# Kernel tuning notes

Hardware: AMD Instinct MI355X
Metric: run time of the kernel (lower is better)

## Reference

```python
import jax, jax.numpy as jnp
import numpy as np

C_REG = 0.1
MAX_ITER = 15
SIGMA = 0.1  # centering parameter for the interior-point steps


def _qp_solve(G, e, h, A, b, max_iter):
    """Batched primal-dual interior-point solver (fixed iteration count, as QPFunction(maxIter=...)).

    Solves per task: min_z 0.5 z^T G z + e^T z  s.t.  z <= h (inequality matrix is identity),  A z = b.
    G: (t,n,n), e,h: (t,n), A: (t,p,n), b: (t,p). Returns z: (t,n).
    """
    t, n = e.shape
    p = A.shape[1]
    dt = G.dtype
    z = jnp.zeros((t, n), dt)
    s = jnp.ones((t, n), dt)    # slack for z + s = h
    lam = jnp.ones((t, n), dt)  # inequality duals
    nu = jnp.zeros((t, p), dt)  # equality duals
    At = jnp.swapaxes(A, 1, 2)              # (t,n,p)
    eye_n = jnp.eye(n, dtype=dt)
    zeros_pp = jnp.zeros((t, p, p), dt)

    def step(carry, _):
        z, s, lam, nu = carry
        # KKT residuals (infeasible-start Newton)
        rz = jnp.einsum('bij,bj->bi', G, z) + e + lam + jnp.einsum('bpi,bp->bi', A, nu)
        rs = z + s - h
        ra = jnp.einsum('bpi,bi->bp', A, z) - b
        mu = jnp.mean(lam * s, axis=1, keepdims=True)
        # eliminate ds and dlam -> reduced saddle system in (dz, dnu)
        r1 = -rz - (lam * rs - lam * s + SIGMA * mu) / s
        D = lam / s  # diagonal of barrier Hessian contribution
        M_top = jnp.concatenate([G + D[:, :, None] * eye_n, At], axis=2)  # (t,n,n+p)
        M_bot = jnp.concatenate([A, zeros_pp], axis=2)                    # (t,p,n+p)
        M = jnp.concatenate([M_top, M_bot], axis=1)                       # (t,n+p,n+p)
        rhs = jnp.concatenate([r1, -ra], axis=1)
        sol = jnp.linalg.solve(M, rhs[..., None])[..., 0]
        dz, dnu = sol[:, :n], sol[:, n:]
        ds = -rs - dz
        dlam = (lam * dz + lam * rs - lam * s + SIGMA * mu) / s
        # fraction-to-boundary step size keeping s, lam > 0
        ratio_s = jnp.where(ds < 0, -s / ds, jnp.inf)
        ratio_l = jnp.where(dlam < 0, -lam / dlam, jnp.inf)
        alpha = jnp.minimum(1.0, 0.99 * jnp.minimum(ratio_s.min(axis=1), ratio_l.min(axis=1)))[:, None]
        return (z + alpha * dz, s + alpha * ds, lam + alpha * dlam, nu + alpha * dnu), None

    (z, s, lam, nu), _ = jax.lax.scan(step, (z, s, lam, nu), xs=None, length=max_iter)
    return z


def setup_inputs() -> dict:
    key = jax.random.key(0)
    k1, k2, k3 = jax.random.split(key, 3)
    tasks, n_way, n_shot, d = 64, 5, 15, 4096
    n_support = n_way * n_shot          # 75
    n_query = 150
    query = jax.random.normal(k1, (tasks, n_query, d), dtype=jnp.float32)
    support = jax.random.normal(k2, (tasks, n_support, d), dtype=jnp.float32)
    support_labels = jax.random.randint(k3, (tasks, n_support), 0, n_way)
    return {"query": query, "support": support, "support_labels": support_labels,
            "n_way": n_way, "n_shot": n_shot}


def reference(query, support, support_labels, n_way, n_shot):
    t, ns, d = support.shape
    nq = query.shape[1]
    n = ns * n_way
    dt = support.dtype
    # linear kernel Gram matrix on support: (t, ns, ns)
    K = jnp.einsum('bnd,bmd->bnm', support, support)
    # block kernel = K kron I_{n_way}, then + I (the module adds 1.0 * eye)
    I_w = jnp.eye(n_way, dtype=dt)
    block_K = (K[:, :, None, :, None] * I_w[None, None, :, None, :]).reshape(t, n, n)
    G = block_K + jnp.eye(n, dtype=dt)
    # one-hot labels, flattened to (t, ns*n_way)
    y1h = jax.nn.one_hot(support_labels, n_way, dtype=dt).reshape(t, n)
    e = -y1h
    h = C_REG * y1h
    # A = I_{ns} kron ones(1, n_way): sums duals over classes per support point
    A = jnp.tile(jnp.eye(ns, dtype=dt)[:, :, None], (1, 1, n_way)).reshape(ns, n)
    A = jnp.broadcast_to(A, (t, ns, n))
    b = jnp.zeros((t, ns), dt)
    z = _qp_solve(G, e, h, A, b, MAX_ITER)
    qp_sol = z.reshape(t, ns, n_way)
    # compatibility = support . query^T : (t, ns, nq); logits = sum over support
    compat = jnp.einsum('bnd,bqd->bnq', support, query)
    logits = jnp.einsum('bnq,bnw->bqw', compat, qp_sol)  # (t, nq, n_way)
    return logits
```

## Files before the change

### kernel.cpp

```cpp
#include <hip/hip_runtime.h>
#include <math.h>

#define T_TASKS 64
#define NS 75
#define NW 5
#define NTOT 375
#define NQ 150
#define DIM 4096
#define QP_ITERS 15
#define SIGMA 0.1f
#define CREG 0.1f

#define OFF_K   0u
#define OFF_W   369664u
#define OFF_Z   2417664u
#define OFF_S   2441664u
#define OFF_LAM 2465664u
#define OFF_NU  2489664u
#define OFF_TV  2494464u

__global__ void qp_init(float* __restrict__ z, float* __restrict__ s,
                        float* __restrict__ lam, float* __restrict__ nu) {
    int idx = blockIdx.x * 256 + threadIdx.x;
    if (idx < T_TASKS * NTOT) { z[idx] = 0.f; s[idx] = 1.f; lam[idx] = 1.f; }
    if (idx < T_TASKS * NS) nu[idx] = 0.f;
}

__global__ __launch_bounds__(256) void gram_partial(const float* __restrict__ support,
                                                    float* __restrict__ Kp) {
    int qd = blockIdx.x, b = blockIdx.y;
    __shared__ __align__(16) float Ss[80 * 132];
    int tid = threadIdx.x;
    int tx = tid & 15, ty = tid >> 4;
    float acc[5][5];
#pragma unroll
    for (int u = 0; u < 5; u++)
#pragma unroll
        for (int v = 0; v < 5; v++) acc[u][v] = 0.f;
    const float* sb = support + (size_t)b * NS * DIM + qd * 1024;
    for (int cc = 0; cc < 8; cc++) {
        __syncthreads();
        for (int idx = tid; idx < 80 * 32; idx += 256) {
            int r = idx >> 5, d4 = idx & 31;
            float4 v = make_float4(0.f, 0.f, 0.f, 0.f);
            if (r < 75) v = *(const float4*)&sb[(size_t)r * DIM + cc * 128 + d4 * 4];
            *(float4*)&Ss[r * 132 + d4 * 4] = v;
        }
        __syncthreads();
        for (int d4 = 0; d4 < 32; d4++) {
            float4 av[5], bv[5];
#pragma unroll
            for (int u = 0; u < 5; u++) av[u] = *(const float4*)&Ss[(ty * 5 + u) * 132 + d4 * 4];
#pragma unroll
            for (int v = 0; v < 5; v++) bv[v] = *(const float4*)&Ss[(tx * 5 + v) * 132 + d4 * 4];
#pragma unroll
            for (int u = 0; u < 5; u++)
#pragma unroll
                for (int v = 0; v < 5; v++)
                    acc[u][v] += av[u].x * bv[v].x + av[u].y * bv[v].y +
                                 av[u].z * bv[v].z + av[u].w * bv[v].w;
        }
    }
    float* Ko = Kp + (size_t)(qd * 64 + b) * 5776;
#pragma unroll
    for (int u = 0; u < 5; u++) {
        int row = ty * 5 + u;
#pragma unroll
        for (int v = 0; v < 5; v++) {
            int col = tx * 5 + v;
            if (row < 75 && col < 75) Ko[row * 76 + col] = acc[u][v];
        }
    }
}

__global__ void gram_reduce(const float* __restrict__ Kp, float* __restrict__ Kg) {
    int idx = blockIdx.x * 256 + threadIdx.x;
    if (idx >= 64 * 5776) return;
    int rc = idx % 5776;
    int row = rc / 76, col = rc % 76;
    float val;
    if (row < 75 && col < 75)
        val = Kp[idx] + Kp[369664 + idx] + Kp[2 * 369664 + idx] + Kp[3 * 369664 + idx];
    else
        val = (row == col) ? 1.f : 0.f;
    Kg[idx] = val;
}

__device__ __forceinline__ void reg_gj80(float (&M)[5][5],
                                         float (*prow)[80], float (*fcol)[80],
                                         int tx, int ty) {
    for (int k = 0; k < 75; k++) {
        int bf = k & 1;
        if (ty == (k & 15)) {
#pragma unroll
            for (int m = 0; m < 5; m++) {
                if (ty + 16 * m == k) {
#pragma unroll
                    for (int n = 0; n < 5; n++) prow[bf][tx + 16 * n] = M[m][n];
                }
            }
        }
        if (tx == (k & 15)) {
#pragma unroll
            for (int n = 0; n < 5; n++) {
                if (tx + 16 * n == k) {
#pragma unroll
                    for (int m = 0; m < 5; m++) fcol[bf][ty + 16 * m] = M[m][n];
                }
            }
        }
        __syncthreads();
        float pinv = 1.f / prow[bf][k];
        float pv[5], fv[5], ps[5];
#pragma unroll
        for (int n = 0; n < 5; n++) {
            pv[n] = prow[bf][tx + 16 * n];
            ps[n] = pv[n] * pinv;
        }
#pragma unroll
        for (int m = 0; m < 5; m++) {
            int r = ty + 16 * m;
            float f = fcol[bf][r] * pinv;
            fv[m] = (r == k) ? 0.f : f;
        }
#pragma unroll
        for (int m = 0; m < 5; m++) {
            int r = ty + 16 * m;
            bool rk = (r == k);
#pragma unroll
            for (int n = 0; n < 5; n++) {
                int c = tx + 16 * n;
                float val = M[m][n] - fv[m] * pv[n];
                val = rk ? ps[n] : val;
                val = (c == k) ? (rk ? pinv : -fv[m]) : val;
                M[m][n] = val;
            }
        }
    }
}

__global__ __launch_bounds__(256) void factor_kernel(
        const float* __restrict__ Kg, const int* __restrict__ labels,
        const float* __restrict__ zg, const float* __restrict__ sg,
        const float* __restrict__ lamg, const float* __restrict__ nug,
        float* __restrict__ Wg, float* __restrict__ tvg) {
    int w = blockIdx.x, b = blockIdx.y;
    int tid = threadIdx.x;
    int tx = tid & 15, ty = tid >> 4;
    __shared__ float prow[2][80], fcol[2][80];
    __shared__ float zw[80], r1w[80], Dv[80], swv[80], lwv[80], nuwv[80];
    __shared__ int labv[80];
    __shared__ float mred[4];

    float M[5][5];
    const float* Kt = Kg + (size_t)b * 5776;
#pragma unroll
    for (int m = 0; m < 5; m++) {
        int r = ty + 16 * m;
#pragma unroll
        for (int n = 0; n < 5; n++) {
            int c = tx + 16 * n;
            M[m][n] = (r < 76 && c < 76) ? Kt[r * 76 + c] : ((r == c) ? 1.f : 0.f);
        }
    }
    if (tid < 80) {
        float zv = 0.f, sv = 1.f, lv = 0.f, nv = 0.f; int lb = -1;
        if (tid < 75) {
            zv = zg[b * NTOT + tid * NW + w];
            sv = sg[b * NTOT + tid * NW + w];
            lv = lamg[b * NTOT + tid * NW + w];
            nv = nug[b * NS + tid];
            lb = labels[b * NS + tid];
        }
        zw[tid] = zv; swv[tid] = sv; lwv[tid] = lv; nuwv[tid] = nv; labv[tid] = lb;
    }
    float part = 0.f;
    for (int idx = tid; idx < NTOT; idx += 256)
        part += lamg[b * NTOT + idx] * sg[b * NTOT + idx];
#pragma unroll
    for (int off = 32; off > 0; off >>= 1) part += __shfl_xor(part, off, 64);
    if ((tid & 63) == 0) mred[tid >> 6] = part;
    __syncthreads();
    float mu = (mred[0] + mred[1] + mred[2] + mred[3]) * (1.f / (float)NTOT);

    float gp[5];
#pragma unroll
    for (int m = 0; m < 5; m++) {
        float a = 0.f;
#pragma unroll
        for (int n = 0; n < 5; n++) a += M[m][n] * zw[tx + 16 * n];
        gp[m] = a;
    }
#pragma unroll
    for (int off = 1; off < 16; off <<= 1)
#pragma unroll
        for (int m = 0; m < 5; m++) gp[m] += __shfl_xor(gp[m], off, 64);
    if (tx == 0) {
#pragma unroll
        for (int m = 0; m < 5; m++) {
            int r = ty + 16 * m;
            float val = 0.f, dv = 0.f;
            if (r < 75) {
                float sv = swv[r], lv = lwv[r], zv = zw[r];
                float e = (labv[r] == w) ? -1.f : 0.f;
                float h = (labv[r] == w) ? CREG : 0.f;
                float rz = gp[m] + zv + e + lv + nuwv[r];
                float rs = zv + sv - h;
                val = -rz - (lv * rs - lv * sv + SIGMA * mu) / sv;
                dv = lv / sv;
            }
            r1w[r] = val; Dv[r] = dv;
        }
    }
    __syncthreads();
    if (tx == ty) {
#pragma unroll
        for (int m = 0; m < 5; m++) {
            int r = ty + 16 * m;
            if (r < 75) M[m][m] += 1.f + Dv[r];
        }
    }

    reg_gj80(M, prow, fcol, tx, ty);

    float* Wo = Wg + (size_t)(b * NW + w) * 6400;
#pragma unroll
    for (int m = 0; m < 5; m++)
#pragma unroll
        for (int n = 0; n < 5; n++)
            Wo[(m * 5 + n) * 256 + tid] = M[m][n];

    float tp[5];
#pragma unroll
    for (int m = 0; m < 5; m++) {
        float a = 0.f;
#pragma unroll
        for (int n = 0; n < 5; n++) a += M[m][n] * r1w[tx + 16 * n];
        tp[m] = a;
    }
#pragma unroll
    for (int off = 1; off < 16; off <<= 1)
#pragma unroll
        for (int m = 0; m < 5; m++) tp[m] += __shfl_xor(tp[m], off, 64);
    if (tx == 0) {
#pragma unroll
        for (int m = 0; m < 5; m++) {
            int r = ty + 16 * m;
            if (r < 75) tvg[(b * NW + w) * 80 + r] = tp[m];
        }
    }
}

__global__ __launch_bounds__(256) void schur_update_kernel(
        const int* __restrict__ labels,
        float* __restrict__ z, float* __restrict__ s,
        float* __restrict__ lam, float* __restrict__ nu,
        const float* __restrict__ Wg, const float* __restrict__ tvg) {
    int b = blockIdx.x;
    int tid = threadIdx.x;
    int tx = tid & 15, ty = tid >> 4;
    __shared__ float prow[2][80], fcol[2][80];
    __shared__ __align__(16) float rhs[80];
    __shared__ __align__(16) float dnu[80];
    __shared__ float mred[4], ared[4];

    float M[5][5];
    const float* Wb = Wg + (size_t)b * NW * 6400;
#pragma unroll
    for (int m = 0; m < 5; m++)
#pragma unroll
        for (int n = 0; n < 5; n++) {
            float a = 0.f;
#pragma unroll
            for (int ww = 0; ww < 5; ww++)
                a += Wb[ww * 6400 + (m * 5 + n) * 256 + tid];
            M[m][n] = a;
        }
    if (tid < 80) {
        float rv = 0.f;
        if (tid < 75) {
#pragma unroll
            for (int ww = 0; ww < 5; ww++)
                rv += z[b * NTOT + tid * NW + ww] + tvg[(b * NW + ww) * 80 + tid];
        }
        rhs[tid] = rv;
    }
    float part = 0.f;
    for (int idx = tid; idx < NTOT; idx += 256)
        part += lam[b * NTOT + idx] * s[b * NTOT + idx];
#pragma unroll
    for (int off = 32; off > 0; off >>= 1) part += __shfl_xor(part, off, 64);
    if ((tid & 63) == 0) mred[tid >> 6] = part;
    __syncthreads();
    float mu = (mred[0] + mred[1] + mred[2] + mred[3]) * (1.f / (float)NTOT);

    reg_gj80(M, prow, fcol, tx, ty);

    float tp[5];
#pragma unroll
    for (int m = 0; m < 5; m++) {
        float a = 0.f;
#pragma unroll
        for (int n = 0; n < 5; n++) a += M[m][n] * rhs[tx + 16 * n];
        tp[m] = a;
    }
#pragma unroll
    for (int off = 1; off < 16; off <<= 1)
#pragma unroll
        for (int m = 0; m < 5; m++) tp[m] += __shfl_xor(tp[m], off, 64);
    if (tx == 0) {
#pragma unroll
        for (int m = 0; m < 5; m++) dnu[ty + 16 * m] = tp[m];
    }
    __syncthreads();

    float rat = INFINITY;
    float dzv[2], dsv[2], dlv[2], zlv[2], slv[2], llv[2];
#pragma unroll
    for (int pass = 0; pass < 2; pass++) {
        int c = tid + 256 * pass;
        dzv[pass] = 0.f; dsv[pass] = 0.f; dlv[pass] = 0.f;
        zlv[pass] = 0.f; slv[pass] = 1.f; llv[pass] = 0.f;
        if (c < NTOT) {
            int i = c / 5, ww = c - (c / 5) * 5;
            int mi = i >> 4, tyi = i & 15;
            const float* Wr = Wb + ww * 6400 + mi * 5 * 256 + tyi * 16;
            const float4* dn4 = (const float4*)dnu;
            float acc = 0.f;
#pragma unroll
            for (int n = 0; n < 5; n++) {
                const float4* w4 = (const float4*)(Wr + n * 256);
#pragma unroll
                for (int q = 0; q < 4; q++) {
                    float4 x = w4[q], y = dn4[4 * n + q];
                    acc += x.x * y.x + x.y * y.y + x.z * y.z + x.w * y.w;
                }
            }
            float tvl = tvg[(b * NW + ww) * 80 + i];
            float zl = z[b * NTOT + c], sl = s[b * NTOT + c], ll = lam[b * NTOT + c];
            float dz_t = tvl - acc;
            int lb = labels[b * NS + i];
            float h = (lb == ww) ? CREG : 0.f;
            float rs = zl + sl - h;
            float ds_t = -rs - dz_t;
            float dl_t = (ll * dz_t + ll * rs - ll * sl + SIGMA * mu) / sl;
            zlv[pass] = zl; slv[pass] = sl; llv[pass] = ll;
            dzv[pass] = dz_t; dsv[pass] = ds_t; dlv[pass] = dl_t;
            float r1 = (ds_t < 0.f) ? (-sl / ds_t) : INFINITY;
            float r2 = (dl_t < 0.f) ? (-ll / dl_t) : INFINITY;
            rat = fminf(rat, fminf(r1, r2));
        }
    }
#pragma unroll
    for (int off = 32; off > 0; off >>= 1) rat = fminf(rat, __shfl_xor(rat, off, 64));
    if ((tid & 63) == 0) ared[tid >> 6] = rat;
    __syncthreads();
    float alpha = fminf(1.f, 0.99f * fminf(fminf(ared[0], ared[1]), fminf(ared[2], ared[3])));
#pragma unroll
    for (int pass = 0; pass < 2; pass++) {
        int c = tid + 256 * pass;
        if (c < NTOT) {
            z[b * NTOT + c]   = zlv[pass] + alpha * dzv[pass];
            s[b * NTOT + c]   = slv[pass] + alpha * dsv[pass];
            lam[b * NTOT + c] = llv[pass] + alpha * dlv[pass];
        }
    }
    if (tid < 75) nu[b * NS + tid] += alpha * dnu[tid];
}

__global__ __launch_bounds__(256) void v_kernel(const float* __restrict__ support,
                                                const float* __restrict__ z,
                                                float* __restrict__ vbuf) {
    int dc = blockIdx.x, b = blockIdx.y;
    __shared__ float zs[NTOT];
    int tid = threadIdx.x;
    for (int idx = tid; idx < NTOT; idx += 256) zs[idx] = z[b * NTOT + idx];
    __syncthreads();
    int d = dc * 256 + tid;
    float acc[5] = {0.f, 0.f, 0.f, 0.f, 0.f};
    const float* sb = support + (size_t)b * NS * DIM + d;
    for (int ss = 0; ss < NS; ss++) {
        float svv = sb[(size_t)ss * DIM];
#pragma unroll
        for (int w = 0; w < 5; w++) acc[w] += svv * zs[ss * 5 + w];
    }
#pragma unroll
    for (int w = 0; w < 5; w++) vbuf[(size_t)(b * NW + w) * DIM + d] = acc[w];
}

__global__ __launch_bounds__(256) void logits_kernel(const float* __restrict__ query,
                                                     const float* __restrict__ vbuf,
                                                     float* __restrict__ out) {
    int qt = blockIdx.x, b = blockIdx.y;
    __shared__ __align__(16) float vs[5 * 1028];
    int tid = threadIdx.x;
    int lane = tid & 63, wid = tid >> 6;
    float acc[8][5];
#pragma unroll
    for (int r = 0; r < 8; r++)
#pragma unroll
        for (int w = 0; w < 5; w++) acc[r][w] = 0.f;

    for (int c = 0; c < 4; c++) {
        __syncthreads();
        for (int idx = tid; idx < 5120; idx += 256) {
            int w = idx >> 10, dd = idx & 1023;
            vs[w * 1028 + dd] = vbuf[(size_t)(b * NW + w) * DIM + c * 1024 + dd];
        }
        __syncthreads();
#pragma unroll
        for (int ri = 0; ri < 8; ri++) {
            int r = wid + ri * 4;
            if (r < 30) {
                int q = qt * 30 + r;
                const float* qp = query + (size_t)(b * NQ + q) * DIM + c * 1024;
#pragma unroll
                for (int j = 0; j < 4; j++) {
                    int d = lane * 4 + j * 256;
                    float4 qv = *(const float4*)(qp + d);
#pragma unroll
                    for (int w = 0; w < 5; w++) {
                        float4 vv = *(const float4*)(&vs[w * 1028 + d]);
                        acc[ri][w] += qv.x * vv.x + qv.y * vv.y + qv.z * vv.z + qv.w * vv.w;
                    }
                }
            }
        }
    }
#pragma unroll
    for (int ri = 0; ri < 8; ri++) {
        int r = wid + ri * 4;
#pragma unroll
        for (int w = 0; w < 5; w++) {
            float v = acc[ri][w];
            for (int off = 32; off > 0; off >>= 1) v += __shfl_xor(v, off, 64);
            if (r < 30 && lane == 0)
                out[(size_t)(b * NQ + qt * 30 + r) * NW + w] = v;
        }
    }
}

extern "C" void kernel_launch(void* const* d_in, const int* in_sizes, int n_in,
                              void* d_out, int out_size, void* d_ws, size_t ws_size,
                              hipStream_t stream) {
    const float* query   = (const float*)d_in[0];
    const float* support = (const float*)d_in[1];
    const int*   labels  = (const int*)d_in[2];
    float* out = (float*)d_out;
    float* ws  = (float*)d_ws;

    float* Kg   = ws + OFF_K;
    float* Wg   = ws + OFF_W;
    float* Kp   = ws + OFF_W;
    float* vbuf = ws + OFF_W;
    float* z    = ws + OFF_Z;
    float* s    = ws + OFF_S;
    float* lam  = ws + OFF_LAM;
    float* nu   = ws + OFF_NU;
    float* tv   = ws + OFF_TV;

    qp_init<<<(T_TASKS * NTOT + 255) / 256, 256, 0, stream>>>(z, s, lam, nu);
    gram_partial<<<dim3(4, T_TASKS), 256, 0, stream>>>(support, Kp);
    gram_reduce<<<(64 * 5776 + 255) / 256, 256, 0, stream>>>(Kp, Kg);
    for (int it = 0; it < QP_ITERS; it++) {
        factor_kernel<<<dim3(NW, T_TASKS), 256, 0, stream>>>(Kg, labels, z, s, lam, nu, Wg, tv);
        schur_update_kernel<<<T_TASKS, 256, 0, stream>>>(labels, z, s, lam, nu, Wg, tv);
    }
    v_kernel<<<dim3(16, T_TASKS), 256, 0, stream>>>(support, z, vbuf);
    logits_kernel<<<dim3(5, T_TASKS), 256, 0, stream>>>(query, vbuf, out);
}
```

Before: 2.167 ms.

## Fuse QP iterations into persistent kernel with grid barrier, atomic Gram accumulation

The 30 per-iteration factor and Schur kernel launches become one persistent kernel of 320 blocks. The blocks synchronise through an atomic-counter grid barrier, so launch gaps between iterations go away. The Gram matrix is now split into 16 depth chunks per task and accumulated with atomicAdd into a pre-initialised buffer, which removes the partial buffer and the reduce kernel. The risks are that the spin barrier requires all 320 blocks to be resident at once, that only one block in five does Schur work between barriers, and that the order of the float atomic additions is not deterministic.

Measured after the change: 6.281 ms. 190% more time.

```diff
diff --git a/kernel.cpp b/kernel.cpp
--- a/kernel.cpp
+++ b/kernel.cpp
@@ -10,6 +10,7 @@
 #define QP_ITERS 15
 #define SIGMA 0.1f
 #define CREG 0.1f
+#define NBLK_QP 320
 
 #define OFF_K   0u
 #define OFF_W   369664u
@@ -18,16 +19,24 @@
 #define OFF_LAM 2465664u
 #define OFF_NU  2489664u
 #define OFF_TV  2494464u
-
-__global__ void qp_init(float* __restrict__ z, float* __restrict__ s,
-                        float* __restrict__ lam, float* __restrict__ nu) {
+#define OFF_BAR (OFF_TV + 75u)
+
+__global__ void init_kernel(float* __restrict__ Kg, float* __restrict__ z,
+                            float* __restrict__ s, float* __restrict__ lam,
+                            float* __restrict__ nu, int* __restrict__ bar) {
     int idx = blockIdx.x * 256 + threadIdx.x;
+    if (idx == 0) bar[0] = 0;
+    if (idx < T_TASKS * 5776) {
+        int rc = idx % 5776;
+        int row = rc / 76, col = rc % 76;
+        Kg[idx] = (row == col && row >= 75) ? 1.f : 0.f;
+    }
     if (idx < T_TASKS * NTOT) { z[idx] = 0.f; s[idx] = 1.f; lam[idx] = 1.f; }
     if (idx < T_TASKS * NS) nu[idx] = 0.f;
 }
 
-__global__ __launch_bounds__(256) void gram_partial(const float* __restrict__ support,
-                                                    float* __restrict__ Kp) {
+__global__ __launch_bounds__(256) void gram_atomic(const float* __restrict__ support,
+                                                   float* __restrict__ Kg) {
     int qd = blockIdx.x, b = blockIdx.y;
     __shared__ __align__(16) float Ss[80 * 132];
     int tid = threadIdx.x;
@@ -37,8 +46,8 @@
     for (int u = 0; u < 5; u++)
 #pragma unroll
         for (int v = 0; v < 5; v++) acc[u][v] = 0.f;
-    const float* sb = support + (size_t)b * NS * DIM + qd * 1024;
-    for (int cc = 0; cc < 8; cc++) {
+    const float* sb = support + (size_t)b * NS * DIM + qd * 256;
+    for (int cc = 0; cc < 2; cc++) {
         __syncthreads();
         for (int idx = tid; idx < 80 * 32; idx += 256) {
             int r = idx >> 5, d4 = idx & 31;
@@ -61,29 +70,16 @@
                                  av[u].z * bv[v].z + av[u].w * bv[v].w;
         }
     }
-    float* Ko = Kp + (size_t)(qd * 64 + b) * 5776;
+    float* Ko = Kg + (size_t)b * 5776;
 #pragma unroll
     for (int u = 0; u < 5; u++) {
         int row = ty * 5 + u;
 #pragma unroll
         for (int v = 0; v < 5; v++) {
             int col = tx * 5 + v;
-            if (row < 75 && col < 75) Ko[row * 76 + col] = acc[u][v];
-        }
-    }
-}
-
-__global__ void gram_reduce(const float* __restrict__ Kp, float* __restrict__ Kg) {
-    int idx = blockIdx.x * 256 + threadIdx.x;
-    if (idx >= 64 * 5776) return;
-    int rc = idx % 5776;
-    int row = rc / 76, col = rc % 76;
-    float val;
-    if (row < 75 && col < 75)
-        val = Kp[idx] + Kp[369664 + idx] + Kp[2 * 369664 + idx] + Kp[3 * 369664 + idx];
-    else
-        val = (row == col) ? 1.f : 0.f;
-    Kg[idx] = val;
+            if (row < 75 && col < 75) atomicAdd(&Ko[row * 76 + col], acc[u][v]);
+        }
+    }
 }
 
 __device__ __forceinline__ void reg_gj80(float (&M)[5][5],
@@ -139,233 +135,246 @@
     }
 }
 
-__global__ __launch_bounds__(256) void factor_kernel(
+__device__ __forceinline__ void grid_barrier(int* bar, int& phase) {
+    __syncthreads();
+    phase++;
+    if (threadIdx.x == 0) {
+        __hip_atomic_fetch_add(bar, 1, __ATOMIC_ACQ_REL, __HIP_MEMORY_SCOPE_AGENT);
+        while (__hip_atomic_load(bar, __ATOMIC_ACQUIRE, __HIP_MEMORY_SCOPE_AGENT)
+               < NBLK_QP * phase)
+            __builtin_amdgcn_s_sleep(2);
+    }
+    __syncthreads();
+}
+
+__global__ __launch_bounds__(256, 2) void qp_loop_kernel(
         const float* __restrict__ Kg, const int* __restrict__ labels,
-        const float* __restrict__ zg, const float* __restrict__ sg,
-        const float* __restrict__ lamg, const float* __restrict__ nug,
-        float* __restrict__ Wg, float* __restrict__ tvg) {
-    int w = blockIdx.x, b = blockIdx.y;
+        float* __restrict__ zg, float* __restrict__ sg,
+        float* __restrict__ lamg, float* __restrict__ nug,
+        float* __restrict__ Wg, float* __restrict__ tvg,
+        int* __restrict__ bar) {
+    int bw = blockIdx.x;
+    int b = bw / NW, w = bw - b * NW;
     int tid = threadIdx.x;
     int tx = tid & 15, ty = tid >> 4;
+
     __shared__ float prow[2][80], fcol[2][80];
     __shared__ float zw[80], r1w[80], Dv[80], swv[80], lwv[80], nuwv[80];
     __shared__ int labv[80];
-    __shared__ float mred[4];
-
-    float M[5][5];
-    const float* Kt = Kg + (size_t)b * 5776;
-#pragma unroll
-    for (int m = 0; m < 5; m++) {
-        int r = ty + 16 * m;
-#pragma unroll
-        for (int n = 0; n < 5; n++) {
-            int c = tx + 16 * n;
-            M[m][n] = (r < 76 && c < 76) ? Kt[r * 76 + c] : ((r == c) ? 1.f : 0.f);
-        }
-    }
-    if (tid < 80) {
-        float zv = 0.f, sv = 1.f, lv = 0.f, nv = 0.f; int lb = -1;
-        if (tid < 75) {
-            zv = zg[b * NTOT + tid * NW + w];
-            sv = sg[b * NTOT + tid * NW + w];
-            lv = lamg[b * NTOT + tid * NW + w];
-            nv = nug[b * NS + tid];
-            lb = labels[b * NS + tid];
-        }
-        zw[tid] = zv; swv[tid] = sv; lwv[tid] = lv; nuwv[tid] = nv; labv[tid] = lb;
-    }
-    float part = 0.f;
-    for (int idx = tid; idx < NTOT; idx += 256)
-        part += lamg[b * NTOT + idx] * sg[b * NTOT + idx];
-#pragma unroll
-    for (int off = 32; off > 0; off >>= 1) part += __shfl_xor(part, off, 64);
-    if ((tid & 63) == 0) mred[tid >> 6] = part;
-    __syncthreads();
-    float mu = (mred[0] + mred[1] + mred[2] + mred[3]) * (1.f / (float)NTOT);
-
-    float gp[5];
-#pragma unroll
-    for (int m = 0; m < 5; m++) {
-        float a = 0.f;
-#pragma unroll
-        for (int n = 0; n < 5; n++) a += M[m][n] * zw[tx + 16 * n];
-        gp[m] = a;
-    }
-#pragma unroll
-    for (int off = 1; off < 16; off <<= 1)
-#pragma unroll
-        for (int m = 0; m < 5; m++) gp[m] += __shfl_xor(gp[m], off, 64);
-    if (tx == 0) {
-#pragma unroll
-        for (int m = 0; m < 5; m++) {
-            int r = ty + 16 * m;
-            float val = 0.f, dv = 0.f;
-            if (r < 75) {
-                float sv = swv[r], lv = lwv[r], zv = zw[r];
-                float e = (labv[r] == w) ? -1.f : 0.f;
-                float h = (labv[r] == w) ? CREG : 0.f;
-                float rz = gp[m] + zv + e + lv + nuwv[r];
-                float rs = zv + sv - h;
-                val = -rz - (lv * rs - lv * sv + SIGMA * mu) / sv;
-                dv = lv / sv;
-            }
-            r1w[r] = val; Dv[r] = dv;
-        }
-    }
-    __syncthreads();
-    if (tx == ty) {
-#pragma unroll
-        for (int m = 0; m < 5; m++) {
-            int r = ty + 16 * m;
-            if (r < 75) M[m][m] += 1.f + Dv[r];
-        }
-    }
-
-    reg_gj80(M, prow, fcol, tx, ty);
-
-    float* Wo = Wg + (size_t)(b * NW + w) * 6400;
-#pragma unroll
-    for (int m = 0; m < 5; m++)
-#pragma unroll
-        for (int n = 0; n < 5; n++)
-            Wo[(m * 5 + n) * 256 + tid] = M[m][n];
-
-    float tp[5];
-#pragma unroll
-    for (int m = 0; m < 5; m++) {
-        float a = 0.f;
-#pragma unroll
-        for (int n = 0; n < 5; n++) a += M[m][n] * r1w[tx + 16 * n];
-        tp[m] = a;
-    }
-#pragma unroll
-    for (int off = 1; off < 16; off <<= 1)
-#pragma unroll
-        for (int m = 0; m < 5; m++) tp[m] += __shfl_xor(tp[m], off, 64);
-    if (tx == 0) {
-#pragma unroll
-        for (int m = 0; m < 5; m++) {
-            int r = ty + 16 * m;
-            if (r < 75) tvg[(b * NW + w) * 80 + r] = tp[m];
-        }
-    }
-}
-
-__global__ __launch_bounds__(256) void schur_update_kernel(
-        const int* __restrict__ labels,
-        float* __restrict__ z, float* __restrict__ s,
-        float* __restrict__ lam, float* __restrict__ nu,
-        const float* __restrict__ Wg, const float* __restrict__ tvg) {
-    int b = blockIdx.x;
-    int tid = threadIdx.x;
-    int tx = tid & 15, ty = tid >> 4;
-    __shared__ float prow[2][80], fcol[2][80];
+    __shared__ float mred[4], ared[4];
     __shared__ __align__(16) float rhs[80];
     __shared__ __align__(16) float dnu[80];
-    __shared__ float mred[4], ared[4];
-
-    float M[5][5];
+
+    const float* Kt = Kg + (size_t)b * 5776;
+    float* Wo = Wg + (size_t)(b * NW + w) * 6400;
     const float* Wb = Wg + (size_t)b * NW * 6400;
-#pragma unroll
-    for (int m = 0; m < 5; m++)
-#pragma unroll
-        for (int n = 0; n < 5; n++) {
-            float a = 0.f;
-#pragma unroll
-            for (int ww = 0; ww < 5; ww++)
-                a += Wb[ww * 6400 + (m * 5 + n) * 256 + tid];
-            M[m][n] = a;
-        }
-    if (tid < 80) {
-        float rv = 0.f;
-        if (tid < 75) {
-#pragma unroll
-            for (int ww = 0; ww < 5; ww++)
-                rv += z[b * NTOT + tid * NW + ww] + tvg[(b * NW + ww) * 80 + tid];
-        }
-        rhs[tid] = rv;
-    }
-    float part = 0.f;
-    for (int idx = tid; idx < NTOT; idx += 256)
-        part += lam[b * NTOT + idx] * s[b * NTOT + idx];
-#pragma unroll
-    for (int off = 32; off > 0; off >>= 1) part += __shfl_xor(part, off, 64);
-    if ((tid & 63) == 0) mred[tid >> 6] = part;
-    __syncthreads();
-    float mu = (mred[0] + mred[1] + mred[2] + mred[3]) * (1.f / (float)NTOT);
-
-    reg_gj80(M, prow, fcol, tx, ty);
-
-    float tp[5];
-#pragma unroll
-    for (int m = 0; m < 5; m++) {
-        float a = 0.f;
-#pragma unroll
-        for (int n = 0; n < 5; n++) a += M[m][n] * rhs[tx + 16 * n];
-        tp[m] = a;
-    }
-#pragma unroll
-    for (int off = 1; off < 16; off <<= 1)
-#pragma unroll
-        for (int m = 0; m < 5; m++) tp[m] += __shfl_xor(tp[m], off, 64);
-    if (tx == 0) {
-#pragma unroll
-        for (int m = 0; m < 5; m++) dnu[ty + 16 * m] = tp[m];
-    }
-    __syncthreads();
-
-    float rat = INFINITY;
-    float dzv[2], dsv[2], dlv[2], zlv[2], slv[2], llv[2];
-#pragma unroll
-    for (int pass = 0; pass < 2; pass++) {
-        int c = tid + 256 * pass;
-        dzv[pass] = 0.f; dsv[pass] = 0.f; dlv[pass] = 0.f;
-        zlv[pass] = 0.f; slv[pass] = 1.f; llv[pass] = 0.f;
-        if (c < NTOT) {
-            int i = c / 5, ww = c - (c / 5) * 5;
-            int mi = i >> 4, tyi = i & 15;
-            const float* Wr = Wb + ww * 6400 + mi * 5 * 256 + tyi * 16;
-            const float4* dn4 = (const float4*)dnu;
-            float acc = 0.f;
-#pragma unroll
-            for (int n = 0; n < 5; n++) {
-                const float4* w4 = (const float4*)(Wr + n * 256);
-#pragma unroll
-                for (int q = 0; q < 4; q++) {
-                    float4 x = w4[q], y = dn4[4 * n + q];
-                    acc += x.x * y.x + x.y * y.y + x.z * y.z + x.w * y.w;
-                }
-            }
-            float tvl = tvg[(b * NW + ww) * 80 + i];
-            float zl = z[b * NTOT + c], sl = s[b * NTOT + c], ll = lam[b * NTOT + c];
-            float dz_t = tvl - acc;
-            int lb = labels[b * NS + i];
-            float h = (lb == ww) ? CREG : 0.f;
-            float rs = zl + sl - h;
-            float ds_t = -rs - dz_t;
-            float dl_t = (ll * dz_t + ll * rs - ll * sl + SIGMA * mu) / sl;
-            zlv[pass] = zl; slv[pass] = sl; llv[pass] = ll;
-            dzv[pass] = dz_t; dsv[pass] = ds_t; dlv[pass] = dl_t;
-            float r1 = (ds_t < 0.f) ? (-sl / ds_t) : INFINITY;
-            float r2 = (dl_t < 0.f) ? (-ll / dl_t) : INFINITY;
-            rat = fminf(rat, fminf(r1, r2));
-        }
-    }
-#pragma unroll
-    for (int off = 32; off > 0; off >>= 1) rat = fminf(rat, __shfl_xor(rat, off, 64));
-    if ((tid & 63) == 0) ared[tid >> 6] = rat;
-    __syncthreads();
-    float alpha = fminf(1.f, 0.99f * fminf(fminf(ared[0], ared[1]), fminf(ared[2], ared[3])));
-#pragma unroll
-    for (int pass = 0; pass < 2; pass++) {
-        int c = tid + 256 * pass;
-        if (c < NTOT) {
-            z[b * NTOT + c]   = zlv[pass] + alpha * dzv[pass];
-            s[b * NTOT + c]   = slv[pass] + alpha * dsv[pass];
-            lam[b * NTOT + c] = llv[pass] + alpha * dlv[pass];
-        }
-    }
-    if (tid < 75) nu[b * NS + tid] += alpha * dnu[tid];
+    int phase = 0;
+
+    for (int it = 0; it < QP_ITERS; it++) {
+        {
+            float M[5][5];
+#pragma unroll
+            for (int m = 0; m < 5; m++) {
+                int r = ty + 16 * m;
+#pragma unroll
+                for (int n = 0; n < 5; n++) {
+                    int c = tx + 16 * n;
+                    M[m][n] = (r < 76 && c < 76) ? Kt[r * 76 + c] : ((r == c) ? 1.f : 0.f);
+                }
+            }
+            if (tid < 80) {
+                float zv = 0.f, sv = 1.f, lv = 0.f, nv = 0.f; int lb = -1;
+                if (tid < 75) {
+                    zv = zg[b * NTOT + tid * NW + w];
+                    sv = sg[b * NTOT + tid * NW + w];
+                    lv = lamg[b * NTOT + tid * NW + w];
+                    nv = nug[b * NS + tid];
+                    lb = labels[b * NS + tid];
+                }
+                zw[tid] = zv; swv[tid] = sv; lwv[tid] = lv; nuwv[tid] = nv; labv[tid] = lb;
+            }
+            float part = 0.f;
+            for (int idx = tid; idx < NTOT; idx += 256)
+                part += lamg[b * NTOT + idx] * sg[b * NTOT + idx];
+#pragma unroll
+            for (int off = 32; off > 0; off >>= 1) part += __shfl_xor(part, off, 64);
+            if ((tid & 63) == 0) mred[tid >> 6] = part;
+            __syncthreads();
+            float mu = (mred[0] + mred[1] + mred[2] + mred[3]) * (1.f / (float)NTOT);
+
+            float gp[5];
+#pragma unroll
+            for (int m = 0; m < 5; m++) {
+                float a = 0.f;
+#pragma unroll
+                for (int n = 0; n < 5; n++) a += M[m][n] * zw[tx + 16 * n];
+                gp[m] = a;
+            }
+#pragma unroll
+            for (int off = 1; off < 16; off <<= 1)
+#pragma unroll
+                for (int m = 0; m < 5; m++) gp[m] += __shfl_xor(gp[m], off, 64);
+            if (tx == 0) {
+#pragma unroll
+                for (int m = 0; m < 5; m++) {
+                    int r = ty + 16 * m;
+                    float val = 0.f, dv = 0.f;
+                    if (r < 75) {
+                        float sv = swv[r], lv = lwv[r], zv = zw[r];
+                        float e = (labv[r] == w) ? -1.f : 0.f;
+                        float h = (labv[r] == w) ? CREG : 0.f;
+                        float rz = gp[m] + zv + e + lv + nuwv[r];
+                        float rs = zv + sv - h;
+                        val = -rz - (lv * rs - lv * sv + SIGMA * mu) / sv;
+                        dv = lv / sv;
+                    }
+                    r1w[r] = val; Dv[r] = dv;
+                }
+            }
+            __syncthreads();
+            if (tx == ty) {
+#pragma unroll
+                for (int m = 0; m < 5; m++) {
+                    int r = ty + 16 * m;
+                    if (r < 75) M[m][m] += 1.f + Dv[r];
+                }
+            }
+
+            reg_gj80(M, prow, fcol, tx, ty);
+
+#pragma unroll
+            for (int m = 0; m < 5; m++)
+#pragma unroll
+                for (int n = 0; n < 5; n++)
+                    Wo[(m * 5 + n) * 256 + tid] = M[m][n];
+
+            float tp[5];
+#pragma unroll
+            for (int m = 0; m < 5; m++) {
+                float a = 0.f;
+#pragma unroll
+                for (int n = 0; n < 5; n++) a += M[m][n] * r1w[tx + 16 * n];
+                tp[m] = a;
+            }
+#pragma unroll
+            for (int off = 1; off < 16; off <<= 1)
+#pragma unroll
+                for (int m = 0; m < 5; m++) tp[m] += __shfl_xor(tp[m], off, 64);
+            if (tx == 0) {
+#pragma unroll
+                for (int m = 0; m < 5; m++) {
+                    int r = ty + 16 * m;
+                    if (r < 75) tvg[(b * NW + w) * 80 + r] = tp[m];
+                }
+            }
+        }
+        grid_barrier(bar, phase);
+
+        if (w == 0) {
+            float M[5][5];
+#pragma unroll
+            for (int m = 0; m < 5; m++)
+#pragma unroll
+                for (int n = 0; n < 5; n++) {
+                    float a = 0.f;
+#pragma unroll
+                    for (int ww = 0; ww < 5; ww++)
+                        a += Wb[ww * 6400 + (m * 5 + n) * 256 + tid];
+                    M[m][n] = a;
+                }
+            if (tid < 80) {
+                float rv = 0.f;
+                if (tid < 75) {
+#pragma unroll
+                    for (int ww = 0; ww < 5; ww++)
+                        rv += zg[b * NTOT + tid * NW + ww] + tvg[(b * NW + ww) * 80 + tid];
+                }
+                rhs[tid] = rv;
+            }
+            float part = 0.f;
+            for (int idx = tid; idx < NTOT; idx += 256)
+                part += lamg[b * NTOT + idx] * sg[b * NTOT + idx];
+#pragma unroll
+            for (int off = 32; off > 0; off >>= 1) part += __shfl_xor(part, off, 64);
+            if ((tid & 63) == 0) mred[tid >> 6] = part;
+            __syncthreads();
+            float mu = (mred[0] + mred[1] + mred[2] + mred[3]) * (1.f / (float)NTOT);
+
+            reg_gj80(M, prow, fcol, tx, ty);
+
+            float tp[5];
+#pragma unroll
+            for (int m = 0; m < 5; m++) {
+                float a = 0.f;
+#pragma unroll
+                for (int n = 0; n < 5; n++) a += M[m][n] * rhs[tx + 16 * n];
+                tp[m] = a;
+            }
+#pragma unroll
+            for (int off = 1; off < 16; off <<= 1)
+#pragma unroll
+                for (int m = 0; m < 5; m++) tp[m] += __shfl_xor(tp[m], off, 64);
+            if (tx == 0) {
+#pragma unroll
+                for (int m = 0; m < 5; m++) dnu[ty + 16 * m] = tp[m];
+            }
+            __syncthreads();
+
+            float rat = INFINITY;
+            float dzv[2], dsv[2], dlv[2], zlv[2], slv[2], llv[2];
+#pragma unroll
+            for (int pass = 0; pass < 2; pass++) {
+                int c = tid + 256 * pass;
+                dzv[pass] = 0.f; dsv[pass] = 0.f; dlv[pass] = 0.f;
+                zlv[pass] = 0.f; slv[pass] = 1.f; llv[pass] = 0.f;
+                if (c < NTOT) {
+                    int i = c / 5, ww = c - (c / 5) * 5;
+                    int mi = i >> 4, tyi = i & 15;
+                    const float* Wr = Wb + ww * 6400 + mi * 5 * 256 + tyi * 16;
+                    const float4* dn4 = (const float4*)dnu;
+                    float acc = 0.f;
+#pragma unroll
+                    for (int n = 0; n < 5; n++) {
+                        const float4* w4 = (const float4*)(Wr + n * 256);
+#pragma unroll
+                        for (int q = 0; q < 4; q++) {
+                            float4 x = w4[q], y = dn4[4 * n + q];
+                            acc += x.x * y.x + x.y * y.y + x.z * y.z + x.w * y.w;
+                        }
+                    }
+                    float tvl = tvg[(b * NW + ww) * 80 + i];
+                    float zl = zg[b * NTOT + c], sl = sg[b * NTOT + c], ll = lamg[b * NTOT + c];
+                    float dz_t = tvl - acc;
+                    int lb = labels[b * NS + i];
+                    float h = (lb == ww) ? CREG : 0.f;
+                    float rs = zl + sl - h;
+                    float ds_t = -rs - dz_t;
+                    float dl_t = (ll * dz_t + ll * rs - ll * sl + SIGMA * mu) / sl;
+                    zlv[pass] = zl; slv[pass] = sl; llv[pass] = ll;
+                    dzv[pass] = dz_t; dsv[pass] = ds_t; dlv[pass] = dl_t;
+                    float r1 = (ds_t < 0.f) ? (-sl / ds_t) : INFINITY;
+                    float r2 = (dl_t < 0.f) ? (-ll / dl_t) : INFINITY;
+                    rat = fminf(rat, fminf(r1, r2));
+                }
+            }
+#pragma unroll
+            for (int off = 32; off > 0; off >>= 1) rat = fminf(rat, __shfl_xor(rat, off, 64));
+            if ((tid & 63) == 0) ared[tid >> 6] = rat;
+            __syncthreads();
+            float alpha = fminf(1.f, 0.99f * fminf(fminf(ared[0], ared[1]), fminf(ared[2], ared[3])));
+#pragma unroll
+            for (int pass = 0; pass < 2; pass++) {
+                int c = tid + 256 * pass;
+                if (c < NTOT) {
+                    zg[b * NTOT + c]   = zlv[pass] + alpha * dzv[pass];
+                    sg[b * NTOT + c]   = slv[pass] + alpha * dsv[pass];
+                    lamg[b * NTOT + c] = llv[pass] + alpha * dlv[pass];
+                }
+            }
+            if (tid < 75) nug[b * NS + tid] += alpha * dnu[tid];
+        }
+        grid_barrier(bar, phase);
+    }
 }
 
 __global__ __launch_bounds__(256) void v_kernel(const float* __restrict__ support,
@@ -451,21 +460,17 @@
 
     float* Kg   = ws + OFF_K;
     float* Wg   = ws + OFF_W;
-    float* Kp   = ws + OFF_W;
     float* vbuf = ws + OFF_W;
     float* z    = ws + OFF_Z;
     float* s    = ws + OFF_S;
     float* lam  = ws + OFF_LAM;
     float* nu   = ws + OFF_NU;
     float* tv   = ws + OFF_TV;
-
-    qp_init<<<(T_TASKS * NTOT + 255) / 256, 256, 0, stream>>>(z, s, lam, nu);
-    gram_partial<<<dim3(4, T_TASKS), 256, 0, stream>>>(support, Kp);
-    gram_reduce<<<(64 * 5776 + 255) / 256, 256, 0, stream>>>(Kp, Kg);
-    for (int it = 0; it < QP_ITERS; it++) {
-        factor_kernel<<<dim3(NW, T_TASKS), 256, 0, stream>>>(Kg, labels, z, s, lam, nu, Wg, tv);
-        schur_update_kernel<<<T_TASKS, 256, 0, stream>>>(labels, z, s, lam, nu, Wg, tv);
-    }
+    int*   bar  = (int*)(ws + OFF_BAR);
+
+    init_kernel<<<(T_TASKS * 5776 + 255) / 256, 256, 0, stream>>>(Kg, z, s, lam, nu, bar);
+    gram_atomic<<<dim3(16, T_TASKS), 256, 0, stream>>>(support, Kg);
+    qp_loop_kernel<<<NBLK_QP, 256, 0, stream>>>(Kg, labels, z, s, lam, nu, Wg, tv, bar);
     v_kernel<<<dim3(16, T_TASKS), 256, 0, stream>>>(support, z, vbuf);
     logits_kernel<<<dim3(5, T_TASKS), 256, 0, stream>>>(query, vbuf, out);
 }
```
